# Optimization experiments

Hardware: AMD Instinct MI355X
Metric: run time of the kernel (lower is better)

The kernel has to match this reference:

```python
import jax, jax.numpy as jnp
import numpy as np

N = 100000   # nodes
E = 800000   # edges per layer
H = 4        # heads
C = 32       # per-head channels (hidden_channels // heads)
IN = 128
HID = H * C  # 128
NEG_SLOPE = 0.2


def gat_layer(x, edge_index, W, att_src, att_dst, bias):
    # PyG GATConv (concat=True, add_self_loops=True)
    n = x.shape[0]
    loop = jnp.arange(n, dtype=edge_index.dtype)
    src = jnp.concatenate([edge_index[0], loop])
    dst = jnp.concatenate([edge_index[1], loop])
    h = (x @ W).reshape(n, H, C)                     # [N,H,C]
    a_src = jnp.sum(h * att_src, axis=-1)            # [N,H]
    a_dst = jnp.sum(h * att_dst, axis=-1)            # [N,H]
    e = jax.nn.leaky_relu(a_src[src] + a_dst[dst], NEG_SLOPE)  # [E',H]
    # segment softmax over incoming edges of each destination node
    m = jax.ops.segment_max(e, dst, num_segments=n)  # [N,H]
    e = jnp.exp(e - m[dst])
    s = jax.ops.segment_sum(e, dst, num_segments=n)  # [N,H]
    alpha = e / (s[dst] + 1e-16)                     # [E',H]
    msg = h[src] * alpha[:, :, None]                 # [E',H,C]
    out = jax.ops.segment_sum(msg, dst, num_segments=n)  # [N,H,C]
    return out.reshape(n, H * C) + bias


def setup_inputs() -> dict:
    key = jax.random.key(0)
    ks = jax.random.split(key, 20)
    inp = {"x": jax.random.normal(ks[0], (N, IN), jnp.float32)}
    dins = [IN, HID, HID]
    for l in range(3):
        din = dins[l]
        inp[f"edge_index{l}"] = jax.random.randint(ks[1 + l], (2, E), 0, N, dtype=jnp.int32)
        inp[f"W{l}"] = jax.random.normal(ks[4 + l], (din, H * C), jnp.float32) / np.sqrt(din)
        inp[f"att_src{l}"] = jax.random.normal(ks[7 + l], (H, C), jnp.float32) * 0.1
        inp[f"att_dst{l}"] = jax.random.normal(ks[10 + l], (H, C), jnp.float32) * 0.1
        inp[f"bias{l}"] = jnp.zeros((H * C,), jnp.float32)
    return inp


def reference(x, edge_index0, edge_index1, edge_index2,
              W0, att_src0, att_dst0, bias0,
              W1, att_src1, att_dst1, bias1,
              W2, att_src2, att_dst2, bias2):
    edges = [edge_index0, edge_index1, edge_index2]
    params = [(W0, att_src0, att_dst0, bias0),
              (W1, att_src1, att_dst1, bias1),
              (W2, att_src2, att_dst2, bias2)]
    for ei, (W, a_s, a_d, b) in zip(edges, params):
        x = jax.nn.relu(gat_layer(x, ei, W, a_s, a_d, b))
    return x
```

## Files before the change

kernel.cpp:

```cpp
#include <hip/hip_runtime.h>
#include <hip/hip_bf16.h>
#include <hip/hip_fp16.h>
#include <type_traits>

#define NNODES 100000
#define NEDGES 800000
#define HIDDIM 128
#define NHEAD 4

#define EPB 2048
#define NBLK 392
#define XCDG 49
#define BSH 7
#define NBUCK 782

typedef _Float16 half8 __attribute__((ext_vector_type(8)));
typedef _Float16 half2t __attribute__((ext_vector_type(2)));
typedef float floatx4 __attribute__((ext_vector_type(4)));


__global__ __launch_bounds__(256) void bucketA_k(const int* __restrict__ e0,
                                                 const int* __restrict__ e1,
                                                 const int* __restrict__ e2,
                                                 int* __restrict__ counts) {
    __shared__ int hist[NBUCK];
    int l = blockIdx.y;
    const int* dst = ((l == 0) ? e0 : (l == 1) ? e1 : e2) + NEDGES;
    int j = blockIdx.x;
    for (int t = threadIdx.x; t < NBUCK; t += 256) hist[t] = 0;
    __syncthreads();
    int base = j * EPB;
    int lim = min(EPB, NEDGES - base);
    if (lim == EPB) {
        #pragma unroll
        for (int it = 0; it < EPB / 256; it++)
            atomicAdd(&hist[dst[base + it * 256 + threadIdx.x] >> BSH], 1);
    } else {
        for (int i = threadIdx.x; i < lim; i += 256)
            atomicAdd(&hist[dst[base + i] >> BSH], 1);
    }
    __syncthreads();
    int* crow = counts + ((size_t)l * NBLK + j) * NBUCK;
    for (int t = threadIdx.x; t < NBUCK; t += 256) crow[t] = hist[t];
}

__global__ __launch_bounds__(256) void bucketB1_k(int* __restrict__ counts,
                                                  int* __restrict__ bucketTotal) {
    __shared__ int part[4][64];
    int l = blockIdx.y;
    int tid = threadIdx.x;
    int wave = tid >> 6;
    int lane = tid & 63;
    int b = blockIdx.x * 64 + lane;
    bool valid = b < NBUCK;
    const int CQ = NBLK / 4;
    int t0 = wave * CQ, t1 = t0 + CQ;
    int sum = 0;
    if (valid) {
        for (int t = t0; t < t1; t++)
            sum += counts[((size_t)l * NBLK + t) * NBUCK + b];
    }
    part[wave][lane] = sum;
    __syncthreads();
    int off = 0;
    for (int w = 0; w < wave; w++) off += part[w][lane];
    if (valid) {
        int run = off;
        for (int t = t0; t < t1; t++) {
            size_t idx = ((size_t)l * NBLK + t) * NBUCK + b;
            int v = counts[idx];
            counts[idx] = run;
            run += v;
        }
        if (wave == 3) bucketTotal[l * NBUCK + b] = run;
    }
}

__global__ __launch_bounds__(1024) void bucketB2_k(const int* __restrict__ bucketTotal,
                                                   int* __restrict__ ebBase,
                                                   int* __restrict__ csrBase) {
    __shared__ int sd[1024];
    int l = blockIdx.x;
    int t = threadIdx.x;
    int tot = (t < NBUCK) ? bucketTotal[l * NBUCK + t] : 0;
    sd[t] = tot;
    __syncthreads();
    for (int off = 1; off < 1024; off <<= 1) {
        int u = (t >= off) ? sd[t - off] : 0;
        __syncthreads();
        sd[t] += u;
        __syncthreads();
    }
    if (t < NBUCK) ebBase[l * NBUCK + t] = sd[t] - tot;
    __syncthreads();
    int nb = (t == NBUCK - 1) ? (NNODES - (NBUCK - 1) * 128) : 128;
    int v2 = (t < NBUCK) ? (tot + nb) : 0;
    sd[t] = v2;
    __syncthreads();
    for (int off = 1; off < 1024; off <<= 1) {
        int u = (t >= off) ? sd[t - off] : 0;
        __syncthreads();
        sd[t] += u;
        __syncthreads();
    }
    if (t < NBUCK) csrBase[l * NBUCK + t] = sd[t] - v2;
}

__global__ __launch_bounds__(256) void bucketC_k(const int* __restrict__ e0,
                                                 const int* __restrict__ e1,
                                                 const int* __restrict__ e2,
                                                 const int* __restrict__ counts,
                                                 const int* __restrict__ ebBase,
                                                 int* __restrict__ edgeBuf) {
    __shared__ int cur[NBUCK];
    int l = blockIdx.y;
    const int* ei = (l == 0) ? e0 : (l == 1) ? e1 : e2;
    const int* src = ei;
    const int* dst = ei + NEDGES;
    int bx = blockIdx.x;
    int j = (bx & 7) * XCDG + (bx >> 3);
    const int* bs = counts + ((size_t)l * NBLK + j) * NBUCK;
    const int* eb = ebBase + l * NBUCK;
    for (int t = threadIdx.x; t < NBUCK; t += 256) cur[t] = eb[t] + bs[t];
    __syncthreads();
    int base = j * EPB;
    int lim = min(EPB, NEDGES - base);
    int* ebuf = edgeBuf + (size_t)l * NEDGES;
    if (lim == EPB) {
        #pragma unroll
        for (int it = 0; it < EPB / 256; it++) {
            int i = it * 256 + threadIdx.x;
            int d = dst[base + i];
            int s = src[base + i];
            int pos = atomicAdd(&cur[d >> BSH], 1);
            ebuf[pos] = ((d & 127) << 17) | s;
        }
    } else {
        for (int i = threadIdx.x; i < lim; i += 256) {
            int d = dst[base + i];
            int s = src[base + i];
            int pos = atomicAdd(&cur[d >> BSH], 1);
            ebuf[pos] = ((d & 127) << 17) | s;
        }
    }
}

__global__ __launch_bounds__(256) void bucketD_k(const int* __restrict__ edgeBuf,
                                                 const int* __restrict__ bucketTotal,
                                                 const int* __restrict__ ebBase,
                                                 const int* __restrict__ csrBase,
                                                 int* __restrict__ offs,
                                                 int* __restrict__ deg,
                                                 int* __restrict__ srcs) {
    __shared__ int cnt[128];
    __shared__ int offl[128];
    __shared__ int cur[128];
    int b = blockIdx.x, l = blockIdx.y;
    int t = threadIdx.x;
    int nb = (b == NBUCK - 1) ? (NNODES - (NBUCK - 1) * 128) : 128;
    int eb0 = ebBase[l * NBUCK + b];
    int ecnt = bucketTotal[l * NBUCK + b];
    int csr0 = csrBase[l * NBUCK + b];
    const int* ebuf = edgeBuf + (size_t)l * NEDGES;
    int* srcsL = srcs + (size_t)l * (NEDGES + NNODES);
    if (t < 128) cnt[t] = 0;
    __syncthreads();
    for (int i = t; i < ecnt; i += 256)
        atomicAdd(&cnt[ebuf[eb0 + i] >> 17], 1);
    __syncthreads();
    if (t < 128) {
        int lane = t & 63;
        int x = cnt[t] + 1;
        #pragma unroll
        for (int o = 1; o < 64; o <<= 1) {
            int u = __shfl_up(x, o);
            if (lane >= o) x += u;
        }
        offl[t] = x;
    }
    __syncthreads();
    if (t < 128) {
        int c = cnt[t];
        int incl = offl[t] + ((t >= 64) ? offl[63] : 0);
        int o = csr0 + incl - (c + 1);
        cur[t] = o;
        if (t < nb) {
            int node = b * 128 + t;
            offs[l * NNODES + node] = o;
            deg[l * NNODES + node] = c;
            srcsL[o + c] = node;
        }
    }
    __syncthreads();
    for (int i = t; i < ecnt; i += 256) {
        int w = ebuf[eb0 + i];
        int pos = atomicAdd(&cur[w >> 17], 1);
        srcsL[pos] = w & 0x1FFFF;
    }
}


template <typename AT>
__global__ __launch_bounds__(256, 2) void gemm_mfma_k(const AT* __restrict__ A,
                                                      const float* __restrict__ B,
                                                      const float* __restrict__ attS,
                                                      const float* __restrict__ attD,
                                                      __half* __restrict__ C16,
                                                      float* __restrict__ aS,
                                                      float* __restrict__ aD, int M) {
    __shared__ __half Bt[144 * 136];
    const int tid = threadIdx.x;
    {
        int kk = (tid & 63) * 2;
        int g = tid >> 6;
        #pragma unroll
        for (int jn = 0; jn < 8; jn++) {
            int n0 = g * 4 + jn * 16;
            float4 r0 = *(const float4*)(B + (size_t)kk * 128 + n0);
            float4 r1 = *(const float4*)(B + (size_t)(kk + 1) * 128 + n0);
            float f0[4] = {r0.x, r0.y, r0.z, r0.w};
            float f1[4] = {r1.x, r1.y, r1.z, r1.w};
            #pragma unroll
            for (int i = 0; i < 4; i++)
                *(__half2*)(&Bt[(n0 + i) * 136 + kk]) = __floats2half2_rn(f0[i], f1[i]);
        }
    }
    if (tid < 128) {
        int k = tid;
        const float* Brow = B + (size_t)k * 128;
        #pragma unroll
        for (int h = 0; h < NHEAD; h++) {
            float s0 = 0.f, s1 = 0.f;
            #pragma unroll 8
            for (int c = 0; c < 32; c++) {
                float bb = Brow[h * 32 + c];
                s0 += bb * attS[h * 32 + c];
                s1 += bb * attD[h * 32 + c];
            }
            Bt[(128 + h * 2 + 0) * 136 + k] = (_Float16)s0;
            Bt[(128 + h * 2 + 1) * 136 + k] = (_Float16)s1;
        }
    } else {
        int k = tid - 128;
        #pragma unroll
        for (int j = 8; j < 16; j++) Bt[(128 + j) * 136 + k] = (_Float16)0.f;
    }
    __syncthreads();

    const int lane = tid & 63;
    const int wave = tid >> 6;
    const int m = lane & 15;
    const int q = lane >> 4;

    half8 bfrag[9][4];
    #pragma unroll
    for (int c = 0; c < 9; c++)
        #pragma unroll
        for (int t = 0; t < 4; t++)
            bfrag[c][t] = *(const half8*)(&Bt[(c * 16 + m) * 136 + t * 32 + q * 8]);

    for (int iter = 0; iter < 4; iter++) {
        int rb = blockIdx.x * 256 + iter * 64 + wave * 16;
        if (rb >= M) break;
        int row = rb + m;
        int rowc = row < M ? row : M - 1;
        half8 a[4];
        if constexpr (std::is_same<AT, __half>::value) {
            const __half* ap = A + (size_t)rowc * HIDDIM;
            #pragma unroll
            for (int t = 0; t < 4; t++)
                a[t] = *(const half8*)(ap + t * 32 + q * 8);
        } else {
            const float* ap = A + (size_t)rowc * HIDDIM;
            #pragma unroll
            for (int t = 0; t < 4; t++) {
                float4 u = *(const float4*)(ap + t * 32 + q * 8);
                float4 v = *(const float4*)(ap + t * 32 + q * 8 + 4);
                half8 h;
                h[0] = (_Float16)u.x; h[1] = (_Float16)u.y;
                h[2] = (_Float16)u.z; h[3] = (_Float16)u.w;
                h[4] = (_Float16)v.x; h[5] = (_Float16)v.y;
                h[6] = (_Float16)v.z; h[7] = (_Float16)v.w;
                a[t] = h;
            }
        }
        floatx4 acc[9];
        #pragma unroll
        for (int c = 0; c < 9; c++) acc[c] = (floatx4){0.f, 0.f, 0.f, 0.f};
        #pragma unroll
        for (int t = 0; t < 4; t++)
            #pragma unroll
            for (int c = 0; c < 9; c++)
                acc[c] = __builtin_amdgcn_mfma_f32_16x16x32_f16(a[t], bfrag[c][t], acc[c], 0, 0, 0);
        #pragma unroll
        for (int c = 0; c < 8; c++)
            #pragma unroll
            for (int r = 0; r < 4; r++) {
                int grow = rb + q * 4 + r;
                if (grow < M)
                    C16[(size_t)grow * HIDDIM + c * 16 + m] = __float2half(acc[c][r]);
            }
        if (m < 8) {
            float* ap = (m & 1) ? aD : aS;
            int head = m >> 1;
            #pragma unroll
            for (int r = 0; r < 4; r++) {
                int grow = rb + q * 4 + r;
                if (grow < M) ap[(size_t)grow * 4 + head] = acc[8][r];
            }
        }
    }
}


template <bool HALF_OUT>
__global__ __launch_bounds__(256) void agg_k(const __half* __restrict__ h16,
                                             const int* __restrict__ offs,
                                             const int* __restrict__ deg,
                                             const int* __restrict__ srcs,
                                             const float* __restrict__ aS,
                                             const float* __restrict__ aD,
                                             const float* __restrict__ bias,
                                             void* __restrict__ outv) {
    int tid = threadIdx.x;
    int lane = tid & 63;
    int grp = lane >> 4;
    int cg = lane & 15;
    int c8 = cg * 8;
    int head = cg >> 2;
    int n = blockIdx.x * 16 + (tid >> 6) * 4 + grp;
    bool nvalid = n < NNODES;
    int nn = nvalid ? n : NNODES - 1;
    int start = offs[nn];
    int cnt = deg[nn] + 1;
    float ad = aD[(size_t)nn * 4 + head];
    half2t acc0[4], acc1[4];
    #pragma unroll
    for (int i = 0; i < 4; i++) {
        acc0[i] = (half2t){(_Float16)0.f, (_Float16)0.f};
        acc1[i] = (half2t){(_Float16)0.f, (_Float16)0.f};
    }
    float wsum = 0.f;
    const int base = grp * 16;

    for (int chunk = 0; chunk < cnt; chunk += 16) {
        int idx = chunk + cg;
        int lim = cnt - chunk;
        int sv = srcs[start + (idx < cnt ? idx : cnt - 1)];
        float asv[16];
        half8 hv[16];
        #pragma unroll
        for (int j = 0; j < 16; j++) {
            int sj = __shfl(sv, base + j);
            asv[j] = aS[(size_t)sj * 4 + head];
            hv[j] = *(const half8*)(h16 + (size_t)sj * HIDDIM + c8);
        }
        #pragma unroll
        for (int j = 0; j < 16; j++) {
            float e = asv[j] + ad;
            e = (e > 0.f) ? e : 0.2f * e;
            float w = (j < lim) ? __expf(e) : 0.f;
            wsum += w;
            _Float16 wh = (_Float16)w;
            half2t w2 = (half2t){wh, wh};
            if ((j & 1) == 0) {
                #pragma unroll
                for (int i = 0; i < 4; i++)
                    acc0[i] += w2 * (half2t){hv[j][2 * i], hv[j][2 * i + 1]};
            } else {
                #pragma unroll
                for (int i = 0; i < 4; i++)
                    acc1[i] += w2 * (half2t){hv[j][2 * i], hv[j][2 * i + 1]};
            }
        }
    }

    if (nvalid) {
        float inv = 1.f / (wsum + 1e-16f);
        float v[8];
        #pragma unroll
        for (int i = 0; i < 4; i++) {
            half2t s = acc0[i] + acc1[i];
            float o0 = (float)s[0] * inv + bias[c8 + 2 * i];
            float o1 = (float)s[1] * inv + bias[c8 + 2 * i + 1];
            v[2 * i] = o0 > 0.f ? o0 : 0.f;
            v[2 * i + 1] = o1 > 0.f ? o1 : 0.f;
        }
        if constexpr (HALF_OUT) {
            union { uint4 u; __half2 h2v[4]; } pk;
            #pragma unroll
            for (int i = 0; i < 4; i++) pk.h2v[i] = __floats2half2_rn(v[2 * i], v[2 * i + 1]);
            *(uint4*)((__half*)outv + (size_t)n * HIDDIM + c8) = pk.u;
        } else {
            float* out = (float*)outv;
            *(float4*)(out + (size_t)n * HIDDIM + c8) = make_float4(v[0], v[1], v[2], v[3]);
            *(float4*)(out + (size_t)n * HIDDIM + c8 + 4) = make_float4(v[4], v[5], v[6], v[7]);
        }
    }
}


extern "C" void kernel_launch(void* const* d_in, const int* in_sizes, int n_in,
                              void* d_out, int out_size, void* d_ws, size_t ws_size,
                              hipStream_t stream) {
    (void)in_sizes; (void)n_in; (void)out_size; (void)ws_size;
    const float* x = (const float*)d_in[0];
    const int* e0 = (const int*)d_in[1];
    const int* e1 = (const int*)d_in[6];
    const int* e2 = (const int*)d_in[11];

    char* ws = (char*)d_ws;
    size_t off = 0;
    auto alloc = [&](size_t bytes) -> void* {
        void* p = ws + off;
        off += (bytes + 255) & ~(size_t)255;
        return p;
    };
    __half* xh      = (__half*)alloc((size_t)NNODES * HIDDIM * 2);
    __half* h16     = (__half*)alloc((size_t)NNODES * HIDDIM * 2);
    float* aS       = (float*)alloc((size_t)NNODES * 4 * 4);
    float* aD       = (float*)alloc((size_t)NNODES * 4 * 4);
    int* deg        = (int*)alloc((size_t)3 * NNODES * 4);
    int* offsArr    = (int*)alloc((size_t)3 * NNODES * 4);
    int* srcs       = (int*)alloc((size_t)3 * (NEDGES + NNODES) * 4);
    int* counts     = (int*)alloc((size_t)3 * NBLK * NBUCK * 4);
    int* bucketTot  = (int*)alloc((size_t)3 * NBUCK * 4);
    int* ebBase     = (int*)alloc((size_t)3 * NBUCK * 4);
    int* csrBase    = (int*)alloc((size_t)3 * NBUCK * 4);
    int* edgeBuf    = (int*)alloc((size_t)3 * NEDGES * 4);

    hipLaunchKernelGGL(bucketA_k, dim3(NBLK, 3), dim3(256), 0, stream, e0, e1, e2, counts);
    hipLaunchKernelGGL(bucketB1_k, dim3((NBUCK + 63) / 64, 3), dim3(256), 0, stream,
                       counts, bucketTot);
    hipLaunchKernelGGL(bucketB2_k, dim3(3), dim3(1024), 0, stream, bucketTot, ebBase, csrBase);
    hipLaunchKernelGGL(bucketC_k, dim3(NBLK, 3), dim3(256), 0, stream,
                       e0, e1, e2, counts, ebBase, edgeBuf);
    hipLaunchKernelGGL(bucketD_k, dim3(NBUCK, 3), dim3(256), 0, stream,
                       edgeBuf, bucketTot, ebBase, csrBase, offsArr, deg, srcs);

    for (int l = 0; l < 3; l++) {
        const float* Wm    = (const float*)d_in[2 + 5 * l];
        const float* attS  = (const float*)d_in[3 + 5 * l];
        const float* attD  = (const float*)d_in[4 + 5 * l];
        const float* biasv = (const float*)d_in[5 + 5 * l];
        const int* offsL = offsArr + l * NNODES;
        const int* degL  = deg + l * NNODES;
        const int* srcsL = srcs + (size_t)l * (NEDGES + NNODES);

        if (l == 0) {
            hipLaunchKernelGGL((gemm_mfma_k<float>), dim3((NNODES + 255) / 256), dim3(256), 0,
                               stream, x, Wm, attS, attD, h16, aS, aD, NNODES);
        } else {
            hipLaunchKernelGGL((gemm_mfma_k<__half>), dim3((NNODES + 255) / 256), dim3(256), 0,
                               stream, xh, Wm, attS, attD, h16, aS, aD, NNODES);
        }
        if (l == 2) {
            hipLaunchKernelGGL((agg_k<false>), dim3((NNODES + 15) / 16), dim3(256), 0, stream,
                               h16, offsL, degL, srcsL, aS, aD, biasv, d_out);
        } else {
            hipLaunchKernelGGL((agg_k<true>), dim3((NNODES + 15) / 16), dim3(256), 0, stream,
                               h16, offsL, degL, srcsL, aS, aD, biasv, (void*)xh);
        }
    }
}
```

Before: 403.7 us.

## Partition features into 16-channel planes and aggregate one node-slice per thread

The GEMM output, attention scalars and intermediate activations move to a planar layout: eight planes of 16 fp16 channels each, with head-major aS/aD. The aggregation kernel now gives each thread one node and one 16-channel plane, with a grid of 8 planes times node groups. It walks the neighbour list sequentially and software-prefetches the next edge, replacing the old 16-lane shuffle-batched chunks. The aim is to shrink the gather working set per plane so it stays L2/MALL resident and to drop padding waste on low-degree nodes. In exchange, srcs and the exp work are repeated 8 times, and per-thread loops diverge on degree.

```diff
diff --git a/kernel.cpp b/kernel.cpp
--- a/kernel.cpp
+++ b/kernel.cpp
@@ -205,7 +205,7 @@
                                                       const float* __restrict__ B,
                                                       const float* __restrict__ attS,
                                                       const float* __restrict__ attD,
-                                                      __half* __restrict__ C16,
+                                                      _Float16* __restrict__ hbuf,
                                                       float* __restrict__ aS,
                                                       float* __restrict__ aD, int M) {
     __shared__ __half Bt[144 * 136];
@@ -266,10 +266,11 @@
         int rowc = row < M ? row : M - 1;
         half8 a[4];
         if constexpr (std::is_same<AT, __half>::value) {
-            const __half* ap = A + (size_t)rowc * HIDDIM;
+            const _Float16* ap = (const _Float16*)A;
             #pragma unroll
             for (int t = 0; t < 4; t++)
-                a[t] = *(const half8*)(ap + t * 32 + q * 8);
+                a[t] = *(const half8*)(ap + ((size_t)(2 * t + (q >> 1)) * NNODES + rowc) * 16
+                                          + (q & 1) * 8);
         } else {
             const float* ap = A + (size_t)rowc * HIDDIM;
             #pragma unroll
@@ -298,7 +299,7 @@
             for (int r = 0; r < 4; r++) {
                 int grow = rb + q * 4 + r;
                 if (grow < M)
-                    C16[(size_t)grow * HIDDIM + c * 16 + m] = __float2half(acc[c][r]);
+                    hbuf[((size_t)c * NNODES + grow) * 16 + m] = (_Float16)acc[c][r];
             }
         if (m < 8) {
             float* ap = (m & 1) ? aD : aS;
@@ -306,7 +307,7 @@
             #pragma unroll
             for (int r = 0; r < 4; r++) {
                 int grow = rb + q * 4 + r;
-                if (grow < M) ap[(size_t)grow * 4 + head] = acc[8][r];
+                if (grow < M) ap[(size_t)head * NNODES + grow] = acc[8][r];
             }
         }
     }
@@ -314,7 +315,7 @@
 
 
 template <bool HALF_OUT>
-__global__ __launch_bounds__(256) void agg_k(const __half* __restrict__ h16,
+__global__ __launch_bounds__(256) void agg_k(const _Float16* __restrict__ hbuf,
                                              const int* __restrict__ offs,
                                              const int* __restrict__ deg,
                                              const int* __restrict__ srcs,
@@ -322,79 +323,80 @@
                                              const float* __restrict__ aD,
                                              const float* __restrict__ bias,
                                              void* __restrict__ outv) {
-    int tid = threadIdx.x;
-    int lane = tid & 63;
-    int grp = lane >> 4;
-    int cg = lane & 15;
-    int c8 = cg * 8;
-    int head = cg >> 2;
-    int n = blockIdx.x * 16 + (tid >> 6) * 4 + grp;
+    int bx = blockIdx.x;
+    int p = bx & 7;
+    int g = bx >> 3;
+    int head = p >> 1;
+    int n = g * 256 + threadIdx.x;
     bool nvalid = n < NNODES;
     int nn = nvalid ? n : NNODES - 1;
     int start = offs[nn];
     int cnt = deg[nn] + 1;
-    float ad = aD[(size_t)nn * 4 + head];
-    half2t acc0[4], acc1[4];
+    float ad = aD[(size_t)head * NNODES + nn];
+    const float* aSp = aS + (size_t)head * NNODES;
+    const _Float16* hb = hbuf + (size_t)p * NNODES * 16;
+
+    half2t acc[8];
     #pragma unroll
-    for (int i = 0; i < 4; i++) {
-        acc0[i] = (half2t){(_Float16)0.f, (_Float16)0.f};
-        acc1[i] = (half2t){(_Float16)0.f, (_Float16)0.f};
-    }
+    for (int i = 0; i < 8; i++) acc[i] = (half2t){(_Float16)0.f, (_Float16)0.f};
     float wsum = 0.f;
-    const int base = grp * 16;
-
-    for (int chunk = 0; chunk < cnt; chunk += 16) {
-        int idx = chunk + cg;
-        int lim = cnt - chunk;
-        int sv = srcs[start + (idx < cnt ? idx : cnt - 1)];
-        float asv[16];
-        half8 hv[16];
-        #pragma unroll
-        for (int j = 0; j < 16; j++) {
-            int sj = __shfl(sv, base + j);
-            asv[j] = aS[(size_t)sj * 4 + head];
-            hv[j] = *(const half8*)(h16 + (size_t)sj * HIDDIM + c8);
-        }
-        #pragma unroll
-        for (int j = 0; j < 16; j++) {
-            float e = asv[j] + ad;
-            e = (e > 0.f) ? e : 0.2f * e;
-            float w = (j < lim) ? __expf(e) : 0.f;
-            wsum += w;
-            _Float16 wh = (_Float16)w;
-            half2t w2 = (half2t){wh, wh};
-            if ((j & 1) == 0) {
-                #pragma unroll
-                for (int i = 0; i < 4; i++)
-                    acc0[i] += w2 * (half2t){hv[j][2 * i], hv[j][2 * i + 1]};
-            } else {
-                #pragma unroll
-                for (int i = 0; i < 4; i++)
-                    acc1[i] += w2 * (half2t){hv[j][2 * i], hv[j][2 * i + 1]};
-            }
-        }
+
+    int s = srcs[start];
+    float as = aSp[s];
+    const _Float16* hp = hb + (size_t)s * 16;
+    half8 hA = *(const half8*)hp;
+    half8 hB = *(const half8*)(hp + 8);
+
+    for (int j = 0;;) {
+        int jn = j + 1;
+        bool more = jn < cnt;
+        int s2 = srcs[start + (more ? jn : j)];
+        float as2 = aSp[s2];
+        const _Float16* hp2 = hb + (size_t)s2 * 16;
+        half8 hA2 = *(const half8*)hp2;
+        half8 hB2 = *(const half8*)(hp2 + 8);
+
+        float e = as + ad;
+        e = (e > 0.f) ? e : 0.2f * e;
+        float w = __expf(e);
+        wsum += w;
+        _Float16 wh = (_Float16)w;
+        half2t w2 = (half2t){wh, wh};
+        #pragma unroll
+        for (int i = 0; i < 4; i++)
+            acc[i] += w2 * (half2t){hA[2 * i], hA[2 * i + 1]};
+        #pragma unroll
+        for (int i = 0; i < 4; i++)
+            acc[4 + i] += w2 * (half2t){hB[2 * i], hB[2 * i + 1]};
+
+        as = as2; hA = hA2; hB = hB2;
+        j = jn;
+        if (!more) break;
     }
 
     if (nvalid) {
         float inv = 1.f / (wsum + 1e-16f);
-        float v[8];
-        #pragma unroll
-        for (int i = 0; i < 4; i++) {
-            half2t s = acc0[i] + acc1[i];
-            float o0 = (float)s[0] * inv + bias[c8 + 2 * i];
-            float o1 = (float)s[1] * inv + bias[c8 + 2 * i + 1];
+        float v[16];
+        #pragma unroll
+        for (int i = 0; i < 8; i++) {
+            float o0 = (float)acc[i][0] * inv + bias[p * 16 + 2 * i];
+            float o1 = (float)acc[i][1] * inv + bias[p * 16 + 2 * i + 1];
             v[2 * i] = o0 > 0.f ? o0 : 0.f;
             v[2 * i + 1] = o1 > 0.f ? o1 : 0.f;
         }
         if constexpr (HALF_OUT) {
-            union { uint4 u; __half2 h2v[4]; } pk;
-            #pragma unroll
-            for (int i = 0; i < 4; i++) pk.h2v[i] = __floats2half2_rn(v[2 * i], v[2 * i + 1]);
-            *(uint4*)((__half*)outv + (size_t)n * HIDDIM + c8) = pk.u;
+            union { uint4 u[2]; __half2 h2v[8]; } pk;
+            #pragma unroll
+            for (int i = 0; i < 8; i++) pk.h2v[i] = __floats2half2_rn(v[2 * i], v[2 * i + 1]);
+            __half* op = (__half*)outv + ((size_t)p * NNODES + n) * 16;
+            *(uint4*)op = pk.u[0];
+            *(uint4*)(op + 8) = pk.u[1];
         } else {
-            float* out = (float*)outv;
-            *(float4*)(out + (size_t)n * HIDDIM + c8) = make_float4(v[0], v[1], v[2], v[3]);
-            *(float4*)(out + (size_t)n * HIDDIM + c8 + 4) = make_float4(v[4], v[5], v[6], v[7]);
+            float* out = (float*)outv + (size_t)n * HIDDIM + p * 16;
+            *(float4*)(out + 0)  = make_float4(v[0], v[1], v[2], v[3]);
+            *(float4*)(out + 4)  = make_float4(v[4], v[5], v[6], v[7]);
+            *(float4*)(out + 8)  = make_float4(v[8], v[9], v[10], v[11]);
+            *(float4*)(out + 12) = make_float4(v[12], v[13], v[14], v[15]);
         }
     }
 }
@@ -417,7 +419,7 @@
         return p;
     };
     __half* xh      = (__half*)alloc((size_t)NNODES * HIDDIM * 2);
-    __half* h16     = (__half*)alloc((size_t)NNODES * HIDDIM * 2);
+    _Float16* hbuf  = (_Float16*)alloc((size_t)NNODES * HIDDIM * 2);
     float* aS       = (float*)alloc((size_t)NNODES * 4 * 4);
     float* aD       = (float*)alloc((size_t)NNODES * 4 * 4);
     int* deg        = (int*)alloc((size_t)3 * NNODES * 4);
@@ -438,6 +440,8 @@
     hipLaunchKernelGGL(bucketD_k, dim3(NBUCK, 3), dim3(256), 0, stream,
                        edgeBuf, bucketTot, ebBase, csrBase, offsArr, deg, srcs);
 
+    const int NDG = (NNODES + 255) / 256;
+
     for (int l = 0; l < 3; l++) {
         const float* Wm    = (const float*)d_in[2 + 5 * l];
         const float* attS  = (const float*)d_in[3 + 5 * l];
@@ -449,17 +453,17 @@
 
         if (l == 0) {
             hipLaunchKernelGGL((gemm_mfma_k<float>), dim3((NNODES + 255) / 256), dim3(256), 0,
-                               stream, x, Wm, attS, attD, h16, aS, aD, NNODES);
+                               stream, x, Wm, attS, attD, hbuf, aS, aD, NNODES);
         } else {
             hipLaunchKernelGGL((gemm_mfma_k<__half>), dim3((NNODES + 255) / 256), dim3(256), 0,
-                               stream, xh, Wm, attS, attD, h16, aS, aD, NNODES);
+                               stream, (const __half*)xh, Wm, attS, attD, hbuf, aS, aD, NNODES);
         }
         if (l == 2) {
-            hipLaunchKernelGGL((agg_k<false>), dim3((NNODES + 15) / 16), dim3(256), 0, stream,
-                               h16, offsL, degL, srcsL, aS, aD, biasv, d_out);
+            hipLaunchKernelGGL((agg_k<false>), dim3(NDG * 8), dim3(256), 0, stream,
+                               hbuf, offsL, degL, srcsL, aS, aD, biasv, d_out);
         } else {
-            hipLaunchKernelGGL((agg_k<true>), dim3((NNODES + 15) / 16), dim3(256), 0, stream,
-                               h16, offsL, degL, srcsL, aS, aD, biasv, (void*)xh);
-        }
-    }
-}
+            hipLaunchKernelGGL((agg_k<true>), dim3(NDG * 8), dim3(256), 0, stream,
+                               hbuf, offsL, degL, srcsL, aS, aD, biasv, (void*)xh);
+        }
+    }
+}
```

After: 580.9 us. 1.44x slower.

## Partition features into per-XCD slabs with work-stealing aggregation

Applied to the files above, without the earlier changes.

Stores node features as eight 16-channel slabs ([slab][node][16]) and attention scores head-major, so that each slab (3.2 MB) can sit in one XCD's L2. The aggregation kernel becomes persistent: blocks read their XCD id, take node groups from that XCD's slab through atomic counters, then steal work from the other slabs. The aim is to cut cross-XCD gather traffic and L2 misses on the random neighbour reads, at the cost of reading the edge lists eight times (once per slab) and adding atomics and barriers per group.

```diff
diff --git a/kernel.cpp b/kernel.cpp
--- a/kernel.cpp
+++ b/kernel.cpp
@@ -13,10 +13,13 @@
 #define XCDG 49
 #define BSH 7
 #define NBUCK 782
+#define NGRP 782
+#define AGG_BLOCKS 2048
 
 typedef _Float16 half8 __attribute__((ext_vector_type(8)));
 typedef _Float16 half2t __attribute__((ext_vector_type(2)));
 typedef float floatx4 __attribute__((ext_vector_type(4)));
+typedef unsigned int uintx4 __attribute__((ext_vector_type(4)));
 
 
 __global__ __launch_bounds__(256) void bucketA_k(const int* __restrict__ e0,
@@ -78,10 +81,12 @@
 
 __global__ __launch_bounds__(1024) void bucketB2_k(const int* __restrict__ bucketTotal,
                                                    int* __restrict__ ebBase,
-                                                   int* __restrict__ csrBase) {
+                                                   int* __restrict__ csrBase,
+                                                   int* __restrict__ aggCtr) {
     __shared__ int sd[1024];
     int l = blockIdx.x;
     int t = threadIdx.x;
+    if (t < 8) aggCtr[l * 8 + t] = 0;
     int tot = (t < NBUCK) ? bucketTotal[l * NBUCK + t] : 0;
     sd[t] = tot;
     __syncthreads();
@@ -205,7 +210,7 @@
                                                       const float* __restrict__ B,
                                                       const float* __restrict__ attS,
                                                       const float* __restrict__ attD,
-                                                      __half* __restrict__ C16,
+                                                      _Float16* __restrict__ hbuf,
                                                       float* __restrict__ aS,
                                                       float* __restrict__ aD, int M) {
     __shared__ __half Bt[144 * 136];
@@ -266,10 +271,11 @@
         int rowc = row < M ? row : M - 1;
         half8 a[4];
         if constexpr (std::is_same<AT, __half>::value) {
-            const __half* ap = A + (size_t)rowc * HIDDIM;
+            const _Float16* ap = (const _Float16*)A;
             #pragma unroll
             for (int t = 0; t < 4; t++)
-                a[t] = *(const half8*)(ap + t * 32 + q * 8);
+                a[t] = *(const half8*)(ap + ((size_t)(2 * t + (q >> 1)) * NNODES + rowc) * 16
+                                          + (q & 1) * 8);
         } else {
             const float* ap = A + (size_t)rowc * HIDDIM;
             #pragma unroll
@@ -298,7 +304,7 @@
             for (int r = 0; r < 4; r++) {
                 int grow = rb + q * 4 + r;
                 if (grow < M)
-                    C16[(size_t)grow * HIDDIM + c * 16 + m] = __float2half(acc[c][r]);
+                    hbuf[((size_t)c * NNODES + grow) * 16 + m] = (_Float16)acc[c][r];
             }
         if (m < 8) {
             float* ap = (m & 1) ? aD : aS;
@@ -306,7 +312,7 @@
             #pragma unroll
             for (int r = 0; r < 4; r++) {
                 int grow = rb + q * 4 + r;
-                if (grow < M) ap[(size_t)grow * 4 + head] = acc[8][r];
+                if (grow < M) ap[(size_t)head * NNODES + grow] = acc[8][r];
             }
         }
     }
@@ -314,87 +320,129 @@
 
 
 template <bool HALF_OUT>
-__global__ __launch_bounds__(256) void agg_k(const __half* __restrict__ h16,
+__device__ __forceinline__ void agg_group(int g, int p, int tid,
+                                          const _Float16* __restrict__ hbuf,
+                                          const int* __restrict__ offs,
+                                          const int* __restrict__ deg,
+                                          const int* __restrict__ srcs,
+                                          const float* __restrict__ aS,
+                                          const float* __restrict__ aD,
+                                          const float* __restrict__ bias,
+                                          void* __restrict__ outv) {
+    int t2 = tid & 1;
+    int n = g * 128 + (tid >> 1);
+    bool nv = n < NNODES;
+    int nn = nv ? n : NNODES - 1;
+    int head = p >> 1;
+    int start = __builtin_nontemporal_load(offs + nn);
+    int cnt = __builtin_nontemporal_load(deg + nn) + 1;
+    float ad = __builtin_nontemporal_load(aD + (size_t)head * NNODES + nn);
+    const float* aSp = aS + (size_t)head * NNODES;
+    const _Float16* hb = hbuf + (size_t)p * NNODES * 16 + t2 * 8;
+
+    half2t acc0[4], acc1[4];
+    #pragma unroll
+    for (int i = 0; i < 4; i++) {
+        acc0[i] = (half2t){(_Float16)0.f, (_Float16)0.f};
+        acc1[i] = (half2t){(_Float16)0.f, (_Float16)0.f};
+    }
+    float wsum = 0.f;
+
+    for (int chunk = 0; chunk < cnt; chunk += 8) {
+        int sj[8];
+        float asj[8];
+        half8 hj[8];
+        #pragma unroll
+        for (int j = 0; j < 8; j++) {
+            int idx = chunk + j;
+            idx = idx < cnt ? idx : cnt - 1;
+            sj[j] = __builtin_nontemporal_load(srcs + start + idx);
+        }
+        #pragma unroll
+        for (int j = 0; j < 8; j++) {
+            asj[j] = aSp[sj[j]];
+            hj[j] = *(const half8*)(hb + (size_t)sj[j] * 16);
+        }
+        #pragma unroll
+        for (int j = 0; j < 8; j++) {
+            float e = asj[j] + ad;
+            e = (e > 0.f) ? e : 0.2f * e;
+            float w = (chunk + j < cnt) ? __expf(e) : 0.f;
+            wsum += w;
+            _Float16 wh = (_Float16)w;
+            half2t w2 = (half2t){wh, wh};
+            if ((j & 1) == 0) {
+                #pragma unroll
+                for (int i = 0; i < 4; i++)
+                    acc0[i] += w2 * (half2t){hj[j][2 * i], hj[j][2 * i + 1]};
+            } else {
+                #pragma unroll
+                for (int i = 0; i < 4; i++)
+                    acc1[i] += w2 * (half2t){hj[j][2 * i], hj[j][2 * i + 1]};
+            }
+        }
+    }
+
+    if (nv) {
+        float inv = 1.f / (wsum + 1e-16f);
+        float v[8];
+        #pragma unroll
+        for (int i = 0; i < 4; i++) {
+            half2t s = acc0[i] + acc1[i];
+            float o0 = (float)s[0] * inv + bias[p * 16 + t2 * 8 + 2 * i];
+            float o1 = (float)s[1] * inv + bias[p * 16 + t2 * 8 + 2 * i + 1];
+            v[2 * i] = o0 > 0.f ? o0 : 0.f;
+            v[2 * i + 1] = o1 > 0.f ? o1 : 0.f;
+        }
+        if constexpr (HALF_OUT) {
+            union { uintx4 u; __half2 h2v[4]; } pk;
+            #pragma unroll
+            for (int i = 0; i < 4; i++) pk.h2v[i] = __floats2half2_rn(v[2 * i], v[2 * i + 1]);
+            uintx4* op = (uintx4*)((__half*)outv + ((size_t)p * NNODES + n) * 16 + t2 * 8);
+            __builtin_nontemporal_store(pk.u, op);
+        } else {
+            float* out = (float*)outv + (size_t)n * HIDDIM + p * 16 + t2 * 8;
+            floatx4 v0 = {v[0], v[1], v[2], v[3]};
+            floatx4 v1 = {v[4], v[5], v[6], v[7]};
+            __builtin_nontemporal_store(v0, (floatx4*)out);
+            __builtin_nontemporal_store(v1, (floatx4*)(out + 4));
+        }
+    }
+}
+
+template <bool HALF_OUT>
+__global__ __launch_bounds__(256) void agg_k(const _Float16* __restrict__ hbuf,
                                              const int* __restrict__ offs,
                                              const int* __restrict__ deg,
                                              const int* __restrict__ srcs,
                                              const float* __restrict__ aS,
                                              const float* __restrict__ aD,
                                              const float* __restrict__ bias,
-                                             void* __restrict__ outv) {
+                                             void* __restrict__ outv,
+                                             int* __restrict__ ctr) {
+    __shared__ int s_g;
     int tid = threadIdx.x;
-    int lane = tid & 63;
-    int grp = lane >> 4;
-    int cg = lane & 15;
-    int c8 = cg * 8;
-    int head = cg >> 2;
-    int n = blockIdx.x * 16 + (tid >> 6) * 4 + grp;
-    bool nvalid = n < NNODES;
-    int nn = nvalid ? n : NNODES - 1;
-    int start = offs[nn];
-    int cnt = deg[nn] + 1;
-    float ad = aD[(size_t)nn * 4 + head];
-    half2t acc0[4], acc1[4];
-    #pragma unroll
-    for (int i = 0; i < 4; i++) {
-        acc0[i] = (half2t){(_Float16)0.f, (_Float16)0.f};
-        acc1[i] = (half2t){(_Float16)0.f, (_Float16)0.f};
-    }
-    float wsum = 0.f;
-    const int base = grp * 16;
-
-    for (int chunk = 0; chunk < cnt; chunk += 16) {
-        int idx = chunk + cg;
-        int lim = cnt - chunk;
-        int sv = srcs[start + (idx < cnt ? idx : cnt - 1)];
-        float asv[16];
-        half8 hv[16];
-        #pragma unroll
-        for (int j = 0; j < 16; j++) {
-            int sj = __shfl(sv, base + j);
-            asv[j] = aS[(size_t)sj * 4 + head];
-            hv[j] = *(const half8*)(h16 + (size_t)sj * HIDDIM + c8);
-        }
-        #pragma unroll
-        for (int j = 0; j < 16; j++) {
-            float e = asv[j] + ad;
-            e = (e > 0.f) ? e : 0.2f * e;
-            float w = (j < lim) ? __expf(e) : 0.f;
-            wsum += w;
-            _Float16 wh = (_Float16)w;
-            half2t w2 = (half2t){wh, wh};
-            if ((j & 1) == 0) {
-                #pragma unroll
-                for (int i = 0; i < 4; i++)
-                    acc0[i] += w2 * (half2t){hv[j][2 * i], hv[j][2 * i + 1]};
-            } else {
-                #pragma unroll
-                for (int i = 0; i < 4; i++)
-                    acc1[i] += w2 * (half2t){hv[j][2 * i], hv[j][2 * i + 1]};
-            }
-        }
-    }
-
-    if (nvalid) {
-        float inv = 1.f / (wsum + 1e-16f);
-        float v[8];
-        #pragma unroll
-        for (int i = 0; i < 4; i++) {
-            half2t s = acc0[i] + acc1[i];
-            float o0 = (float)s[0] * inv + bias[c8 + 2 * i];
-            float o1 = (float)s[1] * inv + bias[c8 + 2 * i + 1];
-            v[2 * i] = o0 > 0.f ? o0 : 0.f;
-            v[2 * i + 1] = o1 > 0.f ? o1 : 0.f;
-        }
-        if constexpr (HALF_OUT) {
-            union { uint4 u; __half2 h2v[4]; } pk;
-            #pragma unroll
-            for (int i = 0; i < 4; i++) pk.h2v[i] = __floats2half2_rn(v[2 * i], v[2 * i + 1]);
-            *(uint4*)((__half*)outv + (size_t)n * HIDDIM + c8) = pk.u;
-        } else {
-            float* out = (float*)outv;
-            *(float4*)(out + (size_t)n * HIDDIM + c8) = make_float4(v[0], v[1], v[2], v[3]);
-            *(float4*)(out + (size_t)n * HIDDIM + c8 + 4) = make_float4(v[4], v[5], v[6], v[7]);
+    int xcd;
+    asm volatile("s_getreg_b32 %0, hwreg(HW_REG_XCC_ID)" : "=s"(xcd));
+    xcd &= 7;
+    for (;;) {
+        if (tid == 0) s_g = atomicAdd(&ctr[xcd], 1);
+        __syncthreads();
+        int g = s_g;
+        __syncthreads();
+        if (g >= NGRP) break;
+        agg_group<HALF_OUT>(g, xcd, tid, hbuf, offs, deg, srcs, aS, aD, bias, outv);
+    }
+    #pragma unroll 1
+    for (int q = 1; q < 8; q++) {
+        int p2 = (xcd + q) & 7;
+        for (;;) {
+            if (tid == 0) s_g = atomicAdd(&ctr[p2], 1);
+            __syncthreads();
+            int g = s_g;
+            __syncthreads();
+            if (g >= NGRP) break;
+            agg_group<HALF_OUT>(g, p2, tid, hbuf, offs, deg, srcs, aS, aD, bias, outv);
         }
     }
 }
@@ -417,7 +465,7 @@
         return p;
     };
     __half* xh      = (__half*)alloc((size_t)NNODES * HIDDIM * 2);
-    __half* h16     = (__half*)alloc((size_t)NNODES * HIDDIM * 2);
+    _Float16* hbuf  = (_Float16*)alloc((size_t)NNODES * HIDDIM * 2);
     float* aS       = (float*)alloc((size_t)NNODES * 4 * 4);
     float* aD       = (float*)alloc((size_t)NNODES * 4 * 4);
     int* deg        = (int*)alloc((size_t)3 * NNODES * 4);
@@ -428,11 +476,13 @@
     int* ebBase     = (int*)alloc((size_t)3 * NBUCK * 4);
     int* csrBase    = (int*)alloc((size_t)3 * NBUCK * 4);
     int* edgeBuf    = (int*)alloc((size_t)3 * NEDGES * 4);
+    int* aggCtr     = (int*)alloc((size_t)24 * 4);
 
     hipLaunchKernelGGL(bucketA_k, dim3(NBLK, 3), dim3(256), 0, stream, e0, e1, e2, counts);
     hipLaunchKernelGGL(bucketB1_k, dim3((NBUCK + 63) / 64, 3), dim3(256), 0, stream,
                        counts, bucketTot);
-    hipLaunchKernelGGL(bucketB2_k, dim3(3), dim3(1024), 0, stream, bucketTot, ebBase, csrBase);
+    hipLaunchKernelGGL(bucketB2_k, dim3(3), dim3(1024), 0, stream,
+                       bucketTot, ebBase, csrBase, aggCtr);
     hipLaunchKernelGGL(bucketC_k, dim3(NBLK, 3), dim3(256), 0, stream,
                        e0, e1, e2, counts, ebBase, edgeBuf);
     hipLaunchKernelGGL(bucketD_k, dim3(NBUCK, 3), dim3(256), 0, stream,
@@ -449,17 +499,17 @@
 
         if (l == 0) {
             hipLaunchKernelGGL((gemm_mfma_k<float>), dim3((NNODES + 255) / 256), dim3(256), 0,
-                               stream, x, Wm, attS, attD, h16, aS, aD, NNODES);
+                               stream, x, Wm, attS, attD, hbuf, aS, aD, NNODES);
         } else {
             hipLaunchKernelGGL((gemm_mfma_k<__half>), dim3((NNODES + 255) / 256), dim3(256), 0,
-                               stream, xh, Wm, attS, attD, h16, aS, aD, NNODES);
+                               stream, (const __half*)xh, Wm, attS, attD, hbuf, aS, aD, NNODES);
         }
         if (l == 2) {
-            hipLaunchKernelGGL((agg_k<false>), dim3((NNODES + 15) / 16), dim3(256), 0, stream,
-                               h16, offsL, degL, srcsL, aS, aD, biasv, d_out);
+            hipLaunchKernelGGL((agg_k<false>), dim3(AGG_BLOCKS), dim3(256), 0, stream,
+                               hbuf, offsL, degL, srcsL, aS, aD, biasv, d_out, aggCtr + l * 8);
         } else {
-            hipLaunchKernelGGL((agg_k<true>), dim3((NNODES + 15) / 16), dim3(256), 0, stream,
-                               h16, offsL, degL, srcsL, aS, aD, biasv, (void*)xh);
-        }
-    }
-}
+            hipLaunchKernelGGL((agg_k<true>), dim3(AGG_BLOCKS), dim3(256), 0, stream,
+                               hbuf, offsL, degL, srcsL, aS, aD, biasv, (void*)xh, aggCtr + l * 8);
+        }
+    }
+}
```

New measurement: 1.149 ms. +184.7%, slower.
